# Performance work log

Measured on AMD Instinct MI355X. Metric: run time of the kernel, lower is better.

Reference implementation:

```python
import jax, jax.numpy as jnp
import numpy as np

K_MAX = 16
SCALE = 1.0 / (32 * 32)


def setup_inputs() -> dict:
    key = jax.random.key(0)
    k1, k2, k3 = jax.random.split(key, 3)
    B, C_in, C_out, H, W = 16, 32, 32, 256, 256
    x = jax.random.normal(k1, (B, C_in, H, W), dtype=jnp.float32)
    weights_real = SCALE * jax.random.normal(k2, (C_in, C_out, K_MAX, K_MAX), dtype=jnp.float32)
    weights_imag = SCALE * jax.random.normal(k3, (C_in, C_out, K_MAX, K_MAX), dtype=jnp.float32)
    return {"x": x, "weights_real": weights_real, "weights_imag": weights_imag}


def reference(x, weights_real, weights_imag):
    B, C, H, W = x.shape
    C_out = weights_real.shape[1]
    k = min(K_MAX, H, W // 2 + 1)
    x_ft = jnp.fft.rfft2(x, norm='ortho')                 # (B, C, H, W//2+1) complex64
    w = (weights_real + 1j * weights_imag)[:, :, :k, :k]  # (C, C_out, k, k)
    # Faithful to original einsum 'bijk,ijkm->bkm' with broadcast over the
    # size-1 i/j slices: sums x_ft over its ROW axis; x_ft's COLUMN index
    # becomes the output-block row index.
    S = jnp.sum(x_ft[:, :, :k, :k], axis=2)               # (B, C, k)  indexed by freq column
    blk = jnp.einsum('bir,iorc->borc', S, w)              # (B, C_out, k, k)
    out_ft = jnp.zeros((B, C_out, H, W // 2 + 1), dtype=x_ft.dtype)
    out_ft = out_ft.at[:, :, :k, :k].set(blk)
    return jnp.fft.irfft2(out_ft, s=(H, W), norm='ortho')
```

## Files before the change

kernel.cpp:

```cpp
#include <hip/hip_runtime.h>
#include <math.h>


#define TWO_PI_OVER_256 0.02454369260617026

__global__ __launch_bounds__(256) void k1_partial(
    const float* __restrict__ x, float* __restrict__ s_part)
{
    __shared__ float twc[256], tws[256];
    __shared__ float gre[64], gim[64];
    __shared__ float Pre[4][256], Pim[4][256];
    __shared__ float red_re[16][16], red_im[16][16];

    const int t = threadIdx.x;
    const int blk = blockIdx.x;
    const int bi = blk >> 2, chunk = blk & 3;
    const int y0 = chunk << 6;

    {
        double a = TWO_PI_OVER_256 * (double)t;
        twc[t] = (float)cos(a);
        tws[t] = (float)sin(a);
    }
    __syncthreads();
    if (t < 64) {
        const int h = y0 + t;
        float gr = 0.f, gi = 0.f;
        #pragma unroll
        for (int u = 0; u < 16; ++u) {
            const int idx = (u * h) & 255;
            gr += twc[idx];
            gi -= tws[idx];
        }
        gre[t] = gr; gim[t] = gi;
    }
    __syncthreads();

    const float* img = x + (size_t)bi * 65536 + (size_t)y0 * 256;
    const int cg = t & 63, rg = t >> 6;
    float4 pr = {0.f,0.f,0.f,0.f}, pi = {0.f,0.f,0.f,0.f};
    #pragma unroll 4
    for (int k = 0; k < 16; ++k) {
        const int hl = rg + (k << 2);
        const float4 xv = *(const float4*)(img + (hl << 8) + (cg << 2));
        const float gr = gre[hl], gi = gim[hl];
        pr.x += gr * xv.x; pr.y += gr * xv.y; pr.z += gr * xv.z; pr.w += gr * xv.w;
        pi.x += gi * xv.x; pi.y += gi * xv.y; pi.z += gi * xv.z; pi.w += gi * xv.w;
    }
    *(float4*)&Pre[rg][cg << 2] = pr;
    *(float4*)&Pim[rg][cg << 2] = pi;
    __syncthreads();

    {
        const int v = t >> 4, j = t & 15;
        float ar = 0.f, ai = 0.f;
        #pragma unroll
        for (int m = 0; m < 16; ++m) {
            const int w = j + (m << 4);
            const float prr = Pre[0][w] + Pre[1][w] + Pre[2][w] + Pre[3][w];
            const float pii = Pim[0][w] + Pim[1][w] + Pim[2][w] + Pim[3][w];
            const int idx = (v * w) & 255;
            const float c = twc[idx], s = tws[idx];
            ar += prr * c + pii * s;
            ai += pii * c - prr * s;
        }
        red_re[v][j] = ar; red_im[v][j] = ai;
    }
    __syncthreads();
    if (t < 16) {
        float ar = 0.f, ai = 0.f;
        #pragma unroll
        for (int j = 0; j < 16; ++j) { ar += red_re[t][j]; ai += red_im[t][j]; }
        float* sp = s_part + (size_t)bi * 128 + chunk * 32;
        sp[t]      = ar * (1.0f / 256.0f);
        sp[t + 16] = ai * (1.0f / 256.0f);
    }
}

__global__ __launch_bounds__(256) void k23_synth(
    const float* __restrict__ wr, const float* __restrict__ wi,
    const float* __restrict__ s_part, float* __restrict__ out)
{
    __shared__ float twc[256], tws[256];
    __shared__ float Sre[32][16], Sim[32][16];
    __shared__ float Br[256], Bi[256];
    __shared__ __align__(16) float coef[64][36];

    const int t = threadIdx.x;
    const int blk = blockIdx.x;
    const int bo = blk >> 2;
    const int y0 = (blk & 3) << 6;
    const int b = bo >> 5, o = bo & 31;

    {
        double a = TWO_PI_OVER_256 * (double)t;
        twc[t] = (float)cos(a);
        tws[t] = (float)sin(a);
    }
    {
        const float* sb = s_part + (size_t)b * 4096;
        #pragma unroll
        for (int e = t; e < 512; e += 256) {
            const int i = e >> 4, u = e & 15;
            const float* p = sb + i * 128 + u;
            Sre[i][u] = p[0] + p[32] + p[64] + p[96];
            Sim[i][u] = p[16] + p[48] + p[80] + p[112];
        }
    }
    __syncthreads();

    {
        const int u = t >> 4;
        float br = 0.f, bim = 0.f;
        const float* wrp = wr + o * 256 + t;
        const float* wip = wi + o * 256 + t;
        #pragma unroll 8
        for (int i = 0; i < 32; ++i) {
            const float a_re = Sre[i][u], a_im = Sim[i][u];
            const float w_re = wrp[i * 8192], w_im = wip[i * 8192];
            br  += a_re * w_re - a_im * w_im;
            bim += a_re * w_im + a_im * w_re;
        }
        Br[t] = br; Bi[t] = bim;
    }
    __syncthreads();

    {
        const int v = t & 15, slot = t >> 4;
        float br[16], bim[16];
        #pragma unroll
        for (int u = 0; u < 16; ++u) { br[u] = Br[u * 16 + v]; bim[u] = Bi[u * 16 + v]; }
        const float scale = (v == 0) ? (1.0f / 256.0f) : (1.0f / 128.0f);
        #pragma unroll
        for (int m = 0; m < 4; ++m) {
            const int r = slot * 4 + m;
            const int y = y0 + r;
            const float c1 = twc[y], s1 = tws[y];
            float gr = br[0], gi = bim[0];
            float cc = 1.f, cs = 0.f;
            #pragma unroll
            for (int u = 1; u < 16; ++u) {
                const float nc = cc * c1 - cs * s1;
                const float ns = cc * s1 + cs * c1;
                cc = nc; cs = ns;
                gr += br[u] * cc - bim[u] * cs;
                gi += br[u] * cs + bim[u] * cc;
            }
            coef[r][v]      = gr * scale;
            coef[r][16 + v] = (v == 0) ? 0.f : (-gi * scale);
        }
    }
    __syncthreads();

    float c[16], s[16];
    #pragma unroll
    for (int v = 0; v < 16; ++v) {
        const int idx = (v * t) & 255;
        c[v] = twc[idx];
        s[v] = tws[idx];
    }
    s[0] = 0.f;

    float* op = out + (size_t)bo * 65536 + (size_t)y0 * 256 + t;
    #pragma unroll 2
    for (int r = 0; r < 64; ++r) {
        const float4* crow = (const float4*)&coef[r][0];
        float acc = 0.f;
        #pragma unroll
        for (int q = 0; q < 4; ++q) {
            const float4 pc = crow[q];
            acc += pc.x * c[q*4+0] + pc.y * c[q*4+1] + pc.z * c[q*4+2] + pc.w * c[q*4+3];
        }
        #pragma unroll
        for (int q = 0; q < 4; ++q) {
            const float4 ps = crow[4+q];
            acc += ps.x * s[q*4+0] + ps.y * s[q*4+1] + ps.z * s[q*4+2] + ps.w * s[q*4+3];
        }
        op[r * 256] = acc;
    }
}

extern "C" void kernel_launch(void* const* d_in, const int* in_sizes, int n_in,
                              void* d_out, int out_size, void* d_ws, size_t ws_size,
                              hipStream_t stream) {
    (void)in_sizes; (void)n_in; (void)out_size; (void)ws_size;
    const float* x  = (const float*)d_in[0];
    const float* wr = (const float*)d_in[1];
    const float* wi = (const float*)d_in[2];
    float* out    = (float*)d_out;
    float* s_part = (float*)d_ws;

    k1_partial<<<2048, 256, 0, stream>>>(x, s_part);
    k23_synth<<<2048, 256, 0, stream>>>(wr, wi, s_part, out);
}
```

Baseline: 283.2 us.

## Precompute twiddle table once and exploit column symmetry in synthesis inverse DFT

Adds a tiny kernel that builds the cos/sin table once in workspace, so the two main kernels load it instead of each block evaluating double-precision cos/sin. The final inverse-DFT row synthesis now has each thread compute 16 rows for one column c0 and emit four columns (c0, c0+64, c0+128, c0+192). It groups the 16 frequencies by v mod 4, so one set of partial sums serves all four outputs through rotation symmetry. This cuts the multiply-adds per output and the coefficient reads from shared memory. In exchange it adds a kernel launch, and each row's stores are split into four strided segments.

New measurement: 259.2 us. 8.5% less time.

```diff
diff --git a/kernel.cpp b/kernel.cpp
--- a/kernel.cpp
+++ b/kernel.cpp
@@ -4,8 +4,17 @@
 
 #define TWO_PI_OVER_256 0.02454369260617026
 
+__global__ __launch_bounds__(256) void k0_tables(float* __restrict__ tbl)
+{
+    const int t = threadIdx.x;
+    const double a = TWO_PI_OVER_256 * (double)t;
+    tbl[t]       = (float)cos(a);
+    tbl[256 + t] = (float)sin(a);
+}
+
 __global__ __launch_bounds__(256) void k1_partial(
-    const float* __restrict__ x, float* __restrict__ s_part)
+    const float* __restrict__ x, const float* __restrict__ tbl,
+    float* __restrict__ s_part)
 {
     __shared__ float twc[256], tws[256];
     __shared__ float gre[64], gim[64];
@@ -17,11 +26,8 @@
     const int bi = blk >> 2, chunk = blk & 3;
     const int y0 = chunk << 6;
 
-    {
-        double a = TWO_PI_OVER_256 * (double)t;
-        twc[t] = (float)cos(a);
-        tws[t] = (float)sin(a);
-    }
+    twc[t] = tbl[t];
+    tws[t] = tbl[256 + t];
     __syncthreads();
     if (t < 64) {
         const int h = y0 + t;
@@ -79,7 +85,8 @@
 
 __global__ __launch_bounds__(256) void k23_synth(
     const float* __restrict__ wr, const float* __restrict__ wi,
-    const float* __restrict__ s_part, float* __restrict__ out)
+    const float* __restrict__ s_part, const float* __restrict__ tbl,
+    float* __restrict__ out)
 {
     __shared__ float twc[256], tws[256];
     __shared__ float Sre[32][16], Sim[32][16];
@@ -92,11 +99,8 @@
     const int y0 = (blk & 3) << 6;
     const int b = bo >> 5, o = bo & 31;
 
-    {
-        double a = TWO_PI_OVER_256 * (double)t;
-        twc[t] = (float)cos(a);
-        tws[t] = (float)sin(a);
-    }
+    twc[t] = tbl[t];
+    tws[t] = tbl[256 + t];
     {
         const float* sb = s_part + (size_t)b * 4096;
         #pragma unroll
@@ -152,32 +156,54 @@
     }
     __syncthreads();
 
-    float c[16], s[16];
+    const int c0 = t & 63, rg = t >> 6;
+    float cv[16], sv[16];
     #pragma unroll
     for (int v = 0; v < 16; ++v) {
-        const int idx = (v * t) & 255;
-        c[v] = twc[idx];
-        s[v] = tws[idx];
-    }
-    s[0] = 0.f;
-
-    float* op = out + (size_t)bo * 65536 + (size_t)y0 * 256 + t;
+        const int idx = (v * c0) & 255;
+        cv[v] = twc[idx];
+        sv[v] = tws[idx];
+    }
+    sv[0] = 0.f;
+
+#define PTERM(ACC, C_, S_, vv) ACC += (C_) * cv[vv] + (S_) * sv[vv];
+#define QTERM(ACC, C_, S_, vv) ACC += (S_) * cv[vv] - (C_) * sv[vv];
+
+    float* op = out + (size_t)bo * 65536 + (size_t)y0 * 256;
     #pragma unroll 2
-    for (int r = 0; r < 64; ++r) {
+    for (int rr = 0; rr < 16; ++rr) {
+        const int r = (rg << 4) + rr;
         const float4* crow = (const float4*)&coef[r][0];
-        float acc = 0.f;
-        #pragma unroll
-        for (int q = 0; q < 4; ++q) {
-            const float4 pc = crow[q];
-            acc += pc.x * c[q*4+0] + pc.y * c[q*4+1] + pc.z * c[q*4+2] + pc.w * c[q*4+3];
-        }
-        #pragma unroll
-        for (int q = 0; q < 4; ++q) {
-            const float4 ps = crow[4+q];
-            acc += ps.x * s[q*4+0] + ps.y * s[q*4+1] + ps.z * s[q*4+2] + ps.w * s[q*4+3];
-        }
-        op[r * 256] = acc;
-    }
+        const float4 pc0 = crow[0], pc1 = crow[1], pc2 = crow[2], pc3 = crow[3];
+        const float4 ps0 = crow[4], ps1 = crow[5], ps2 = crow[6], ps3 = crow[7];
+        float P0 = 0.f, P1 = 0.f, P2 = 0.f, P3 = 0.f, Q1 = 0.f, Q3 = 0.f;
+        PTERM(P0, pc0.x, ps0.x, 0)
+        PTERM(P1, pc0.y, ps0.y, 1)   QTERM(Q1, pc0.y, ps0.y, 1)
+        PTERM(P2, pc0.z, ps0.z, 2)
+        PTERM(P3, pc0.w, ps0.w, 3)   QTERM(Q3, pc0.w, ps0.w, 3)
+        PTERM(P0, pc1.x, ps1.x, 4)
+        PTERM(P1, pc1.y, ps1.y, 5)   QTERM(Q1, pc1.y, ps1.y, 5)
+        PTERM(P2, pc1.z, ps1.z, 6)
+        PTERM(P3, pc1.w, ps1.w, 7)   QTERM(Q3, pc1.w, ps1.w, 7)
+        PTERM(P0, pc2.x, ps2.x, 8)
+        PTERM(P1, pc2.y, ps2.y, 9)   QTERM(Q1, pc2.y, ps2.y, 9)
+        PTERM(P2, pc2.z, ps2.z, 10)
+        PTERM(P3, pc2.w, ps2.w, 11)  QTERM(Q3, pc2.w, ps2.w, 11)
+        PTERM(P0, pc3.x, ps3.x, 12)
+        PTERM(P1, pc3.y, ps3.y, 13)  QTERM(Q1, pc3.y, ps3.y, 13)
+        PTERM(P2, pc3.z, ps3.z, 14)
+        PTERM(P3, pc3.w, ps3.w, 15)  QTERM(Q3, pc3.w, ps3.w, 15)
+
+        const float e02 = P0 + P2, o13 = P1 + P3;
+        const float d02 = P0 - P2, dq  = Q1 - Q3;
+        float* row = op + (r << 8) + c0;
+        row[0]   = e02 + o13;
+        row[64]  = d02 + dq;
+        row[128] = e02 - o13;
+        row[192] = d02 - dq;
+    }
+#undef PTERM
+#undef QTERM
 }
 
 extern "C" void kernel_launch(void* const* d_in, const int* in_sizes, int n_in,
@@ -189,7 +215,9 @@
     const float* wi = (const float*)d_in[2];
     float* out    = (float*)d_out;
     float* s_part = (float*)d_ws;
-
-    k1_partial<<<2048, 256, 0, stream>>>(x, s_part);
-    k23_synth<<<2048, 256, 0, stream>>>(wr, wi, s_part, out);
-}
+    float* tbl    = s_part + 65536;
+
+    k0_tables<<<1, 256, 0, stream>>>(tbl);
+    k1_partial<<<2048, 256, 0, stream>>>(x, tbl, s_part);
+    k23_synth<<<2048, 256, 0, stream>>>(wr, wi, s_part, tbl, out);
+}
```
